# Optimization experiments

Hardware: AMD Instinct MI355X
Metric: run time of the kernel (lower is better)

Reference implementation:

```python
import jax, jax.numpy as jnp
from jax import lax
import numpy as np

B = 2; C = 128; H = 128; W = 128; NPIX = H * W
HTH = 184; HTW = 180; NBINS = HTH * HTW
NSPH = 16384; KHT = 8; KSPH = 16
N0, N1, N2 = 1024, 256, 64
K0, K1, K2 = 8, 8, 8
EPS = 1e-5


def setup_inputs() -> dict:
    key = jax.random.key(0)
    ks = jax.random.split(key, 24)
    f32 = jnp.float32
    inp = {}
    inp["image"] = jax.random.normal(ks[0], (B, C, H, W), f32)
    inp["bn_gamma"] = jnp.ones((C,), f32)
    inp["bn_beta"] = jnp.zeros((C,), f32)
    inp["ht_idx"] = jax.random.randint(ks[1], (NBINS, KHT), 0, NPIX, jnp.int32)
    inp["ht_w"] = jax.random.uniform(ks[2], (NBINS, KHT), f32)
    inp["w_htconv"] = jax.random.normal(ks[3], (3, 3, C, C), f32) / np.sqrt(9.0 * C)
    inp["htbn_gamma"] = jnp.ones((C,), f32)
    inp["htbn_beta"] = jnp.zeros((C,), f32)
    inp["sph_idx"] = jax.random.randint(ks[4], (NSPH, KSPH), 0, NBINS, jnp.int32)
    inp["sph_w"] = jax.random.uniform(ks[5], (NSPH, KSPH), f32)
    inp["w_sc"] = jax.random.normal(ks[6], (3, 64, C), f32) / np.sqrt(1.0 * C)
    inp["b_sc"] = jnp.zeros((3, 64), f32)
    inp["scbn_gamma"] = jnp.ones((3, 64), f32)
    inp["scbn_beta"] = jnp.zeros((3, 64), f32)
    inp["dgcn_w"] = jax.random.normal(ks[7], (3, 4, 128, 64), f32) / np.sqrt(128.0)
    inp["dgcn_b"] = jnp.zeros((3, 4, 64), f32)
    inp["dgcn_hw"] = jax.random.normal(ks[8], (3, 64), f32) / 8.0
    inp["dgcn_hb"] = jnp.zeros((3,), f32)
    inp["ind0"] = jax.random.randint(ks[9], (B, N0), 0, NSPH, jnp.int32)
    inp["ind1"] = jax.random.randint(ks[10], (B, 3, N1), 0, NSPH, jnp.int32)
    inp["ind2"] = jax.random.randint(ks[11], (B, 3, N2), 0, NSPH, jnp.int32)
    # kNN-style edges: structured centers (each node repeated k times), random neighbors
    c0 = jnp.tile(jnp.repeat(jnp.arange(N0, dtype=jnp.int32), K0)[None], (B, 1))
    inp["edge0"] = jnp.stack([c0, jax.random.randint(ks[12], (B, N0 * K0), 0, N0, jnp.int32)], 1)
    c1 = jnp.broadcast_to(jnp.repeat(jnp.arange(N1, dtype=jnp.int32), K1)[None, None], (B, 3, N1 * K1))
    inp["edge1"] = jnp.stack([c1, jax.random.randint(ks[13], (B, 3, N1 * K1), 0, N1, jnp.int32)], 2)
    c2 = jnp.broadcast_to(jnp.repeat(jnp.arange(N2, dtype=jnp.int32), K2)[None, None], (B, 3, N2 * K2))
    inp["edge2"] = jnp.stack([c2, jax.random.randint(ks[14], (B, 3, N2 * K2), 0, N2, jnp.int32)], 2)
    inp["target0"] = jax.random.randint(ks[15], (B, N0), 0, 2, jnp.int32)
    inp["target1"] = jax.random.randint(ks[16], (B * 3, N1), 0, 2, jnp.int32)
    inp["target2"] = jax.random.randint(ks[17], (B * 3, N2), 0, 2, jnp.int32)
    return inp


def _bn2d(x, g, b):
    m = x.mean((0, 2, 3), keepdims=True)
    v = x.var((0, 2, 3), keepdims=True)
    return g[None, :, None, None] * (x - m) * lax.rsqrt(v + EPS) + b[None, :, None, None]


def _sphere(x_htf, sph_idx, sph_w, ind):
    # x_htf: [B,C,NBINS]; ind: [B,S] -> weighted gather of HT bins per sphere node
    mi = sph_idx[ind]          # [B,S,K]
    mw = sph_w[ind]            # [B,S,K]
    g = jax.vmap(lambda xb, ib: xb[:, ib])(x_htf, mi)   # [B,C,S,K]
    return (g * mw[:, None]).sum(-1)                    # [B,C,S]


def _sconv(x, w, b, g, be):
    # 1x1 conv [B,C,S]->[B,64,S] + BN1d (batch stats) + ReLU
    y = jnp.einsum('oc,bcs->bos', w, x) + b[None, :, None]
    m = y.mean((0, 2), keepdims=True)
    v = y.var((0, 2), keepdims=True)
    return jax.nn.relu(g[None, :, None] * (y - m) * lax.rsqrt(v + EPS) + be[None, :, None])


def _dgcn(x, edge, ws, bs, hw, hb, n, k):
    # x: [Bg,n,64]; edge: [Bg,2,n*k] (row0=center, row1=neighbor); 4 EdgeConv layers
    for i in range(4):
        xc = jnp.take_along_axis(x, edge[:, 0, :, None], axis=1)   # [Bg,n*k,Cin]
        xn = jnp.take_along_axis(x, edge[:, 1, :, None], axis=1)
        h = jax.nn.relu(jnp.concatenate([xc, xn - xc], -1) @ ws[i] + bs[i])
        x = h.reshape(x.shape[0], n, k, -1).max(2)                 # max over neighbors
    return x @ hw + hb                                             # [Bg,n] logits


def _bce(logits, target):
    t = target.astype(logits.dtype)
    l = jnp.maximum(logits, 0.0) - logits * t + jnp.log1p(jnp.exp(-jnp.abs(logits)))
    pos = t > 0.5
    npos = jnp.maximum(pos.sum(), 1).astype(l.dtype)
    nneg = jnp.maximum((~pos).sum(), 1).astype(l.dtype)
    return jnp.where(pos, l, 0.0).sum() / npos, jnp.where(pos, 0.0, l).sum() / nneg


def _forward(image, bn_gamma, bn_beta, ht_idx, ht_w, w_htconv, htbn_gamma, htbn_beta,
             sph_idx, sph_w, w_sc, b_sc, scbn_gamma, scbn_beta,
             dgcn_w, dgcn_b, dgcn_hw, dgcn_hb,
             ind0, ind1, ind2, edge0, edge1, edge2, target0, target1, target2):
    x = jax.nn.relu(_bn2d(image, bn_gamma, bn_beta))
    xf = x.reshape(B, C, NPIX)
    # Hough voting: each HT bin accumulates KHT weighted pixels
    ht = (xf[:, :, ht_idx] * ht_w).sum(-1).reshape(B, C, HTH, HTW)
    hc = lax.conv_general_dilated(ht, w_htconv, (1, 1), 'SAME',
                                  dimension_numbers=('NCHW', 'HWIO', 'NCHW'))
    x_htf = jax.nn.relu(_bn2d(hc, htbn_gamma, htbn_beta)).reshape(B, C, NBINS)

    # scale 0
    x0 = _sconv(_sphere(x_htf, sph_idx, sph_w, ind0),
                w_sc[0], b_sc[0], scbn_gamma[0], scbn_beta[0]).transpose(0, 2, 1)
    x0 = _dgcn(x0, edge0, dgcn_w[0], dgcn_b[0], dgcn_hw[0], dgcn_hb[0], N0, K0)   # [B,N0]
    # scale 1 (3 vanishing-point branches folded into batch)
    x1 = _sconv(_sphere(x_htf, sph_idx, sph_w, ind1.reshape(B, -1)),
                w_sc[1], b_sc[1], scbn_gamma[1], scbn_beta[1]).transpose(0, 2, 1)
    x1 = _dgcn(x1.reshape(B * 3, N1, 64), edge1.reshape(B * 3, 2, N1 * K1),
               dgcn_w[1], dgcn_b[1], dgcn_hw[1], dgcn_hb[1], N1, K1)              # [B*3,N1]
    # scale 2
    x2 = _sconv(_sphere(x_htf, sph_idx, sph_w, ind2.reshape(B, -1)),
                w_sc[2], b_sc[2], scbn_gamma[2], scbn_beta[2]).transpose(0, 2, 1)
    x2 = _dgcn(x2.reshape(B * 3, N2, 64), edge2.reshape(B * 3, 2, N2 * K2),
               dgcn_w[2], dgcn_b[2], dgcn_hw[2], dgcn_hb[2], N2, K2)              # [B*3,N2]

    lp0, ln0 = _bce(x0, target0)
    lp1, ln1 = _bce(x1, target1)
    lp2, ln2 = _bce(x2, target2)
    losses = jnp.stack([lp0, ln0, lp1, ln1, lp2, ln2])
    preds = jnp.concatenate([jax.nn.sigmoid(x0).reshape(B, -1),
                             jax.nn.sigmoid(x1).reshape(B, -1),
                             jax.nn.sigmoid(x2).reshape(B, -1)], axis=1)
    return losses, preds


def reference(image, bn_gamma, bn_beta, ht_idx, ht_w, w_htconv, htbn_gamma, htbn_beta,
              sph_idx, sph_w, w_sc, b_sc, scbn_gamma, scbn_beta,
              dgcn_w, dgcn_b, dgcn_hw, dgcn_hb,
              ind0, ind1, ind2, edge0, edge1, edge2, target0, target1, target2):
    return _forward(image, bn_gamma, bn_beta, ht_idx, ht_w, w_htconv, htbn_gamma, htbn_beta,
                    sph_idx, sph_w, w_sc, b_sc, scbn_gamma, scbn_beta,
                    dgcn_w, dgcn_b, dgcn_hw, dgcn_hb,
                    ind0, ind1, ind2, edge0, edge1, edge2, target0, target1, target2)
```

## Files before the change

### kernel.cpp

```cpp
#include <hip/hip_runtime.h>
#include <math.h>

#define B_ 2
#define C_ 128
#define NPIX_ 16384
#define HTH_ 184
#define HTW_ 180
#define NBINS_ 33120
#define PH_ 186
#define PW_ 184
#define NPB_ 1984
#define TOTN_ 3968
#define EPS_ 1e-5f

#define ST_HC_SUM 0
#define ST_HC_SQ  128
#define ST_SC_SUM 256
#define ST_SC_SQ  448
#define ST_LOSS   640
#define ST_IMG_S1 1472
#define ST_IMG_S2 1600

typedef __attribute__((ext_vector_type(8))) short v8s;
typedef __attribute__((ext_vector_type(4))) float v4f;

__device__ inline unsigned short f2b(float f) {
  unsigned u = __builtin_bit_cast(unsigned, f);
  unsigned r = u + 0x7fffu + ((u >> 16) & 1u);
  return (unsigned short)(r >> 16);
}
__device__ inline float b2f(unsigned short u) {
  unsigned v = ((unsigned)u) << 16;
  return __builtin_bit_cast(float, v);
}

__global__ void kprep0(const float* __restrict__ w, const float* __restrict__ dw,
                       unsigned short* __restrict__ wtb, unsigned short* __restrict__ dwb,
                       unsigned* __restrict__ htb2, const float* __restrict__ img,
                       float* __restrict__ st) {
  int bid = blockIdx.x;
  int tid = threadIdx.x;
  if (bid < 1516) {
    int idx = bid*256 + tid;
    if (idx < 147456) {
      int tap = idx >> 14, z = idx & 16383;
      int j = z & 7, lane = (z >> 3) & 63, nt = (z >> 9) & 7, kt = (z >> 12) & 3;
      int l = lane & 15, q = lane >> 4;
      int co = nt*16 + l, ci = kt*32 + q*8 + j;
      wtb[idx] = f2b(w[(tap*C_ + ci)*C_ + co]);
    } else if (idx < 245760) {
      int i2 = idx - 147456;
      int sl = i2 >> 13, z = i2 & 8191;
      int j = z & 7, lane = (z >> 3) & 63, nt = (z >> 9) & 3, kt = (z >> 11) & 3;
      int l = lane & 15, q = lane >> 4;
      int co = nt*16 + l, cc = kt*32 + q*8 + j;
      dwb[i2] = f2b(dw[(sl*128 + cc)*64 + co]);
    } else if (idx < 388096) {
      int i = idx - 245760;
      int d = i & 63;
      int cell = i >> 6;
      int b = cell / 1112, j = cell % 1112;
      int y, x;
      if (j < 184) { y = 0; x = j; }
      else if (j < 368) { y = 185; x = j - 184; }
      else { int c = j - 368; int xi = c / 186; y = c % 186; x = xi == 0 ? 0 : 180 + xi; }
      htb2[((size_t)(b*PH_ + y)*PW_ + x)*64 + d] = 0u;
    }
  } else {
    int kb = bid - 1516;
    int c = kb >> 3, chunk = kb & 7;
    float s1 = 0.f, s2 = 0.f;
    for (int i = chunk*4096 + tid; i < (chunk+1)*4096; i += 256) {
      int b = i >> 14, p = i & (NPIX_-1);
      float v = img[((size_t)(b*C_ + c))*NPIX_ + p];
      s1 += v; s2 += v*v;
    }
    __shared__ float r1[256], r2[256];
    r1[tid] = s1; r2[tid] = s2; __syncthreads();
    for (int off = 128; off; off >>= 1) {
      if (tid < off) { r1[tid] += r1[tid+off]; r2[tid] += r2[tid+off]; }
      __syncthreads();
    }
    if (tid == 0) {
      atomicAdd(&st[ST_IMG_S1 + c], r1[0]);
      atomicAdd(&st[ST_IMG_S2 + c], r2[0]);
    }
  }
}

__global__ void k2_bnrelu_t(const float* __restrict__ img, const float* __restrict__ st,
                            const float* __restrict__ g, const float* __restrict__ be,
                            unsigned short* __restrict__ xt) {
  __shared__ float tile[32*65];
  __shared__ float ash[32], dsh[32];
  int p0 = blockIdx.x*64, c0 = blockIdx.y*32, b = blockIdx.z;
  int tid = threadIdx.x;
  if (tid < 32) {
    int c = c0 + tid;
    float n = (float)(B_*NPIX_);
    float m = st[ST_IMG_S1+c]/n;
    float var = st[ST_IMG_S2+c]/n - m*m;
    float a = g[c]*rsqrtf(var + EPS_);
    ash[tid] = a; dsh[tid] = be[c] - a*m;
  }
  __syncthreads();
  for (int r = 0; r < 8; r++) {
    int flat = tid + r*256;
    int row = flat >> 6, col = flat & 63;
    float v = img[((size_t)(b*C_ + c0 + row))*NPIX_ + p0 + col];
    tile[row*65 + col] = fmaxf(ash[row]*v + dsh[row], 0.f);
  }
  __syncthreads();
  for (int r = 0; r < 4; r++) {
    int flat = (tid + r*256)*2;
    int pl = flat >> 5, cl = flat & 31;
    unsigned lo = f2b(tile[cl*65 + pl]);
    unsigned hi = f2b(tile[(cl+1)*65 + pl]);
    *(unsigned*)&xt[((size_t)b*NPIX_ + p0 + pl)*C_ + c0 + cl] = lo | (hi << 16);
  }
}

__global__ void k3_hough(const unsigned* __restrict__ xt2, const int* __restrict__ hidx,
                         const float* __restrict__ hwt, unsigned* __restrict__ htb2) {
  int tid = threadIdx.x;
  int wv = __builtin_amdgcn_readfirstlane(tid >> 6);
  int bin = blockIdx.x*4 + wv;
  int b = blockIdx.y;
  int lane = tid & 63;
  const unsigned* base = xt2 + (size_t)b*NPIX_*64 + lane;
  float acc0 = 0.f, acc1 = 0.f;
  #pragma unroll
  for (int k = 0; k < 8; k++) {
    int p = hidx[bin*8 + k];
    float w = hwt[bin*8 + k];
    unsigned dv = base[(size_t)p*64];
    acc0 += w * b2f((unsigned short)(dv & 0xffff));
    acc1 += w * b2f((unsigned short)(dv >> 16));
  }
  int y = bin / HTW_, x = bin - y*HTW_;
  unsigned lo = f2b(acc0), hi = f2b(acc1);
  htb2[((size_t)(b*PH_ + y + 1)*PW_ + (x+1))*64 + lane] = lo | (hi << 16);
}

__global__ __launch_bounds__(256, 3) void k4_mfma(
    const unsigned short* __restrict__ htb, const unsigned short* __restrict__ wtb,
    unsigned short* __restrict__ hcb, float* __restrict__ st) {
  __shared__ char smem[32768];
  int tid = threadIdx.x;
  int wav = tid >> 6, lane = tid & 63;
  int quad = lane >> 4, l16 = lane & 15;
  int b = blockIdx.y;
  int p0 = blockIdx.x*128 + wav*32;
  size_t ab[2];
  #pragma unroll
  for (int t = 0; t < 2; t++) {
    int px = p0 + t*16 + l16; if (px > NBINS_-1) px = NBINS_-1;
    int y = px / HTW_, x = px % HTW_;
    ab[t] = (((size_t)(b*PH_ + y))*PW_ + x)*C_ + quad*8;
  }
  v4f acc[2][8];
  #pragma unroll
  for (int t = 0; t < 2; t++)
    #pragma unroll
    for (int nt = 0; nt < 8; nt++) acc[t][nt] = (v4f){0,0,0,0};

  for (int tap = 0; tap < 9; tap++) {
    __syncthreads();
    const uint4* src = (const uint4*)(wtb + tap*16384);
    uint4* dst = (uint4*)smem;
    #pragma unroll
    for (int s = 0; s < 8; s++) dst[tid + s*256] = src[tid + s*256];
    __syncthreads();
    int dy = tap/3, dx = tap - dy*3;
    int toff = (dy*PW_ + dx)*C_;
    v8s a[2][4];
    #pragma unroll
    for (int t = 0; t < 2; t++)
      #pragma unroll
      for (int kt = 0; kt < 4; kt++)
        a[t][kt] = *(const v8s*)&htb[ab[t] + toff + kt*32];
    #pragma unroll
    for (int kt = 0; kt < 4; kt++) {
      #pragma unroll
      for (int nt = 0; nt < 8; nt++) {
        v8s bf = *(const v8s*)(smem + ((((kt*8 + nt)*64) + lane) << 4));
        acc[0][nt] = __builtin_amdgcn_mfma_f32_16x16x32_bf16(a[0][kt], bf, acc[0][nt], 0, 0, 0);
        acc[1][nt] = __builtin_amdgcn_mfma_f32_16x16x32_bf16(a[1][kt], bf, acc[1][nt], 0, 0, 0);
      }
    }
  }
  __syncthreads();
  float* red = (float*)smem;
  float s1[8], s2[8];
  #pragma unroll
  for (int nt = 0; nt < 8; nt++) { s1[nt] = 0.f; s2[nt] = 0.f; }
  #pragma unroll
  for (int t = 0; t < 2; t++) {
    int pbase = p0 + t*16 + quad*4;
    #pragma unroll
    for (int nt = 0; nt < 8; nt++) {
      int co = nt*16 + l16;
      #pragma unroll
      for (int reg = 0; reg < 4; reg++) {
        int po = pbase + reg;
        if (po < NBINS_) {
          float v = acc[t][nt][reg];
          hcb[((size_t)b*NBINS_ + po)*C_ + co] = f2b(v);
          s1[nt] += v; s2[nt] += v*v;
        }
      }
    }
  }
  int slot = wav*4 + quad;
  #pragma unroll
  for (int nt = 0; nt < 8; nt++) red[(nt*16 + l16)*17 + slot] = s1[nt];
  __syncthreads();
  if (tid < 128) {
    float s = 0.f;
    #pragma unroll
    for (int k = 0; k < 16; k++) s += red[tid*17 + k];
    atomicAdd(&st[ST_HC_SUM + tid], s);
  }
  __syncthreads();
  #pragma unroll
  for (int nt = 0; nt < 8; nt++) red[(nt*16 + l16)*17 + slot] = s2[nt];
  __syncthreads();
  if (tid < 128) {
    float s = 0.f;
    #pragma unroll
    for (int k = 0; k < 16; k++) s += red[tid*17 + k];
    atomicAdd(&st[ST_HC_SQ + tid], s);
  }
}

__global__ __launch_bounds__(256) void k67_sphconv(
    const unsigned* __restrict__ hcb2, const float* __restrict__ g, const float* __restrict__ be,
    const int* __restrict__ sph_idx, const float* __restrict__ sph_w,
    const int* __restrict__ ind0, const int* __restrict__ ind1, const int* __restrict__ ind2,
    const float* __restrict__ w_sc, const float* __restrict__ b_sc,
    float* __restrict__ y, float* __restrict__ st) {
  __shared__ float xs[32*128];
  __shared__ float wT[128*65];
  __shared__ float red[256];
  int tid = threadIdx.x;
  int gn0 = blockIdx.x*32;
  int nb0 = gn0 % NPB_;
  int s = nb0 < 1024 ? 0 : (nb0 < 1792 ? 1 : 2);
  int wv = tid >> 6, lane = tid & 63;
  {
    int c0 = lane*2, c1 = c0 + 1;
    float n = (float)(B_*NBINS_);
    float m0 = st[ST_HC_SUM + c0]/n, m1 = st[ST_HC_SUM + c1]/n;
    float va0 = st[ST_HC_SQ + c0]/n - m0*m0, va1 = st[ST_HC_SQ + c1]/n - m1*m1;
    float a0 = g[c0]*rsqrtf(va0 + EPS_), a1 = g[c1]*rsqrtf(va1 + EPS_);
    float d0 = be[c0] - a0*m0, d1 = be[c1] - a1*m1;
    for (int i = 0; i < 8; i++) {
      int node_l = wv*8 + i;
      int gn = gn0 + node_l;
      int b = gn / NPB_, nb = gn % NPB_;
      int v;
      if (nb < 1024) v = ind0[b*1024 + nb];
      else if (nb < 1792) v = ind1[b*768 + nb - 1024];
      else v = ind2[b*192 + nb - 1792];
      v = __builtin_amdgcn_readfirstlane(v);
      const unsigned* base = hcb2 + (size_t)b*NBINS_*64 + lane;
      float acc0 = 0.f, acc1 = 0.f;
      #pragma unroll
      for (int k = 0; k < 16; k++) {
        int mi = sph_idx[v*16 + k];
        float mw = sph_w[v*16 + k];
        unsigned dv = base[(size_t)mi*64];
        acc0 += mw * fmaxf(a0*b2f((unsigned short)(dv & 0xffff)) + d0, 0.f);
        acc1 += mw * fmaxf(a1*b2f((unsigned short)(dv >> 16)) + d1, 0.f);
      }
      *(float2*)&xs[node_l*128 + c0] = make_float2(acc0, acc1);
    }
  }
  for (int r = 0; r < 32; r++) {
    int flat = tid + r*256;
    int o = flat >> 7, cc = flat & 127;
    wT[cc*65 + o] = w_sc[(s*64 + o)*C_ + cc];
  }
  __syncthreads();
  int o = tid & 63, nl = tid >> 6;
  float bias = b_sc[s*64 + o];
  float acc[8];
  #pragma unroll
  for (int i = 0; i < 8; i++) acc[i] = bias;
  for (int cc = 0; cc < 128; cc++) {
    float wvv = wT[cc*65 + o];
    #pragma unroll
    for (int i = 0; i < 8; i++)
      acc[i] += xs[(nl*8 + i)*128 + cc] * wvv;
  }
  float s1 = 0.f, s2 = 0.f;
  #pragma unroll
  for (int i = 0; i < 8; i++) {
    y[(size_t)(gn0 + nl*8 + i)*64 + o] = acc[i];
    s1 += acc[i]; s2 += acc[i]*acc[i];
  }
  red[tid] = s1; __syncthreads();
  if (nl == 0) atomicAdd(&st[ST_SC_SUM + s*64 + o], red[o] + red[64+o] + red[128+o] + red[192+o]);
  __syncthreads();
  red[tid] = s2; __syncthreads();
  if (nl == 0) atomicAdd(&st[ST_SC_SQ + s*64 + o], red[o] + red[64+o] + red[128+o] + red[192+o]);
}

__global__ __launch_bounds__(256) void k10_dgcn(
    const void* __restrict__ xin_, unsigned short* __restrict__ xout,
    const int* __restrict__ edge0, const int* __restrict__ edge1, const int* __restrict__ edge2,
    const unsigned short* __restrict__ dwb, const float* __restrict__ db,
    const float* __restrict__ st, const float* __restrict__ scg, const float* __restrict__ scb,
    int layer, int usebn) {
  __shared__ unsigned short E[128*136];
  __shared__ float ash[64], dsh[64];
  int tid = threadIdx.x;
  int bid = blockIdx.x;
  int s, node_base, le_blk, span; const int* ec;
  if (bid < 128) {
    s = 0; int b = bid >> 6; node_base = b*NPB_; le_blk = (bid & 63)*128;
    span = 8192; ec = edge0 + b*2*8192;
  } else if (bid < 224) {
    int j = bid - 128; s = 1; int seg = j >> 4; int b = seg/3, vp = seg%3;
    node_base = b*NPB_ + 1024 + vp*256; le_blk = (j & 15)*128;
    span = 2048; ec = edge1 + ((b*3+vp)*2)*2048;
  } else {
    int j = bid - 224; s = 2; int seg = j >> 2; int b = seg/3, vp = seg%3;
    node_base = b*NPB_ + 1792 + vp*64; le_blk = (j & 3)*128;
    span = 512; ec = edge2 + ((b*3+vp)*2)*512;
  }
  const int* en = ec + span;
  if (usebn) {
    if (tid < 64) {
      float n = s==0 ? 2048.f : (s==1 ? 1536.f : 384.f);
      float m = st[ST_SC_SUM + s*64 + tid]/n;
      float var = st[ST_SC_SQ + s*64 + tid]/n - m*m;
      float a = scg[s*64 + tid]*rsqrtf(var + EPS_);
      ash[tid] = a; dsh[tid] = scb[s*64 + tid] - a*m;
    }
    __syncthreads();
  }
  {
    int r = tid >> 1, h = tid & 1;
    int e = le_blk + r;
    int ci = ec[e], ni = en[e];
    if (usebn) {
      const float* xc = (const float*)xin_ + (size_t)(node_base + ci)*64;
      const float* xn = (const float*)xin_ + (size_t)(node_base + ni)*64;
      #pragma unroll
      for (int c8 = 0; c8 < 64; c8 += 8) {
        v8s pk;
        #pragma unroll
        for (int j = 0; j < 8; j++) {
          int c = c8 + j;
          float vc = fmaxf(ash[c]*xc[c] + dsh[c], 0.f);
          float val = vc;
          if (h) val = fmaxf(ash[c]*xn[c] + dsh[c], 0.f) - vc;
          pk[j] = (short)f2b(val);
        }
        *(v8s*)&E[r*136 + h*64 + c8] = pk;
      }
    } else {
      const unsigned short* xc = (const unsigned short*)xin_ + (size_t)(node_base + ci)*64;
      const unsigned short* xn = (const unsigned short*)xin_ + (size_t)(node_base + ni)*64;
      #pragma unroll
      for (int c8 = 0; c8 < 64; c8 += 8) {
        v8s vc8 = *(const v8s*)&xc[c8];
        v8s pk = vc8;
        if (h) {
          v8s vn8 = *(const v8s*)&xn[c8];
          #pragma unroll
          for (int j = 0; j < 8; j++)
            pk[j] = (short)f2b(b2f((unsigned short)vn8[j]) - b2f((unsigned short)vc8[j]));
        }
        *(v8s*)&E[r*136 + h*64 + c8] = pk;
      }
    }
  }
  __syncthreads();
  int wave = tid >> 6, lane = tid & 63;
  int quad = lane >> 4, l16 = lane & 15;
  const unsigned short* wb = dwb + (size_t)(s*4 + layer)*8192;
  v4f acc[2][4];
  #pragma unroll
  for (int t = 0; t < 2; t++)
    #pragma unroll
    for (int nt = 0; nt < 4; nt++) acc[t][nt] = (v4f){0,0,0,0};
  #pragma unroll
  for (int kt = 0; kt < 4; kt++) {
    v8s a0 = *(const v8s*)&E[(wave*32 + l16)*136 + quad*8 + kt*32];
    v8s a1 = *(const v8s*)&E[(wave*32 + 16 + l16)*136 + quad*8 + kt*32];
    #pragma unroll
    for (int nt = 0; nt < 4; nt++) {
      v8s bf = *(const v8s*)&wb[((kt*4 + nt)*64 + lane)*8];
      acc[0][nt] = __builtin_amdgcn_mfma_f32_16x16x32_bf16(a0, bf, acc[0][nt], 0, 0, 0);
      acc[1][nt] = __builtin_amdgcn_mfma_f32_16x16x32_bf16(a1, bf, acc[1][nt], 0, 0, 0);
    }
  }
  int vb0 = le_blk/8 + wave*4;
  #pragma unroll
  for (int t = 0; t < 2; t++) {
    #pragma unroll
    for (int nt = 0; nt < 4; nt++) {
      float bias = db[(s*4 + layer)*64 + nt*16 + l16];
      float m = fmaxf(fmaxf(acc[t][nt][0], acc[t][nt][1]),
                      fmaxf(acc[t][nt][2], acc[t][nt][3]));
      m = fmaxf(m + bias, 0.f);
      float other = __shfl_xor(m, 16);
      m = fmaxf(m, other);
      if ((quad & 1) == 0) {
        int v = vb0 + t*2 + (quad >> 1);
        xout[(size_t)(node_base + v)*64 + nt*16 + l16] = f2b(m);
      }
    }
  }
}

__global__ __launch_bounds__(256) void k11_head(
    const unsigned short* __restrict__ x, const float* __restrict__ hw, const float* __restrict__ hb,
    const int* __restrict__ t0, const int* __restrict__ t1, const int* __restrict__ t2,
    float* __restrict__ out, float* __restrict__ st) {
  __shared__ float shw[192];
  int tid = threadIdx.x;
  if (tid < 192) shw[tid] = hw[tid];
  __syncthreads();
  int gn = blockIdx.x*256 + tid;
  bool valid = gn < TOTN_;
  int g = valid ? gn : TOTN_-1;
  int b = g / NPB_, nb = g % NPB_;
  int s, tg;
  if (nb < 1024) { s = 0; tg = t0[b*1024 + nb]; }
  else if (nb < 1792) { s = 1; int j = nb-1024; tg = t1[(b*3 + (j>>8))*256 + (j&255)]; }
  else { s = 2; int j = nb-1792; tg = t2[(b*3 + (j>>6))*64 + (j&63)]; }
  const unsigned short* row = x + (size_t)g*64;
  float logit = hb[s];
  #pragma unroll
  for (int c8 = 0; c8 < 64; c8 += 8) {
    v8s v = *(const v8s*)&row[c8];
    #pragma unroll
    for (int j = 0; j < 8; j++)
      logit += b2f((unsigned short)v[j]) * shw[s*64 + c8 + j];
  }
  if (valid) out[6 + gn] = 1.f / (1.f + expf(-logit));
  float tf = (float)tg;
  float l = fmaxf(logit, 0.f) - logit*tf + log1pf(expf(-fabsf(logit)));
  float sp = (valid && tg) ? l : 0.f;
  float sn = (valid && !tg) ? l : 0.f;
  float cp = (valid && tg) ? 1.f : 0.f;
  float cn = (valid && !tg) ? 1.f : 0.f;
  for (int off = 32; off; off >>= 1) {
    sp += __shfl_down(sp, off);
    sn += __shfl_down(sn, off);
    cp += __shfl_down(cp, off);
    cn += __shfl_down(cn, off);
  }
  if ((tid & 63) == 0) {
    atomicAdd(&st[ST_LOSS + s*4 + 0], sp);
    atomicAdd(&st[ST_LOSS + s*4 + 1], sn);
    atomicAdd(&st[ST_LOSS + s*4 + 2], cp);
    atomicAdd(&st[ST_LOSS + s*4 + 3], cn);
  }
}

__global__ void k12_fin(const float* __restrict__ st, float* __restrict__ out) {
  int i = threadIdx.x;
  if (i < 6) {
    int s = i >> 1; int pos = !(i & 1);
    float sum = st[ST_LOSS + s*4 + (pos ? 0 : 1)];
    float cnt = st[ST_LOSS + s*4 + (pos ? 2 : 3)];
    out[i] = sum / fmaxf(cnt, 1.f);
  }
}

extern "C" void kernel_launch(void* const* d_in, const int* in_sizes, int n_in,
                              void* d_out, int out_size, void* d_ws, size_t ws_size,
                              hipStream_t stream) {
  const float* image  = (const float*)d_in[0];
  const float* bn_g   = (const float*)d_in[1];
  const float* bn_b   = (const float*)d_in[2];
  const int*   ht_idx = (const int*)  d_in[3];
  const float* ht_w   = (const float*)d_in[4];
  const float* w_conv = (const float*)d_in[5];
  const float* htbn_g = (const float*)d_in[6];
  const float* htbn_b = (const float*)d_in[7];
  const int*   sph_idx= (const int*)  d_in[8];
  const float* sph_w  = (const float*)d_in[9];
  const float* w_sc   = (const float*)d_in[10];
  const float* b_sc   = (const float*)d_in[11];
  const float* scbn_g = (const float*)d_in[12];
  const float* scbn_b = (const float*)d_in[13];
  const float* dgcn_w = (const float*)d_in[14];
  const float* dgcn_b = (const float*)d_in[15];
  const float* dgcn_hw= (const float*)d_in[16];
  const float* dgcn_hb= (const float*)d_in[17];
  const int*   ind0   = (const int*)  d_in[18];
  const int*   ind1   = (const int*)  d_in[19];
  const int*   ind2   = (const int*)  d_in[20];
  const int*   edge0  = (const int*)  d_in[21];
  const int*   edge1  = (const int*)  d_in[22];
  const int*   edge2  = (const int*)  d_in[23];
  const int*   t0     = (const int*)  d_in[24];
  const int*   t1     = (const int*)  d_in[25];
  const int*   t2     = (const int*)  d_in[26];
  float* out = (float*)d_out;

  char* ws = (char*)d_ws;
  unsigned short* x_t   = (unsigned short*)(ws);
  unsigned short* htb   = (unsigned short*)(ws +  8388608);
  unsigned short* hcb   = (unsigned short*)(ws + 25911296);
  unsigned short* wtb   = (unsigned short*)(ws + 42868736);
  unsigned short* dwb   = (unsigned short*)(ws + 43163648);
  float*          y_sc  = (float*)(ws + 43360256);
  unsigned short* xdgA  = (unsigned short*)(ws + 44376064);
  unsigned short* xdgB  = (unsigned short*)(ws + 44883968);
  float*          st    = (float*)(ws + 45391872);

  hipMemsetAsync(st, 0, 1728*sizeof(float), stream);
  kprep0<<<2540, 256, 0, stream>>>(w_conv, dgcn_w, wtb, dwb, (unsigned*)htb, image, st);
  k2_bnrelu_t<<<dim3(256,4,2), 256, 0, stream>>>(image, st, bn_g, bn_b, x_t);
  k3_hough<<<dim3(NBINS_/4, B_), 256, 0, stream>>>((const unsigned*)x_t, ht_idx, ht_w, (unsigned*)htb);
  k4_mfma<<<dim3(259, 2), 256, 0, stream>>>(htb, wtb, hcb, st);
  k67_sphconv<<<TOTN_/32, 256, 0, stream>>>((const unsigned*)hcb, htbn_g, htbn_b, sph_idx, sph_w,
                                            ind0, ind1, ind2, w_sc, b_sc, y_sc, st);
  k10_dgcn<<<248, 256, 0, stream>>>((const void*)y_sc, xdgA, edge0, edge1, edge2, dwb, dgcn_b, st, scbn_g, scbn_b, 0, 1);
  k10_dgcn<<<248, 256, 0, stream>>>((const void*)xdgA, xdgB, edge0, edge1, edge2, dwb, dgcn_b, st, scbn_g, scbn_b, 1, 0);
  k10_dgcn<<<248, 256, 0, stream>>>((const void*)xdgB, xdgA, edge0, edge1, edge2, dwb, dgcn_b, st, scbn_g, scbn_b, 2, 0);
  k10_dgcn<<<248, 256, 0, stream>>>((const void*)xdgA, xdgB, edge0, edge1, edge2, dwb, dgcn_b, st, scbn_g, scbn_b, 3, 0);
  k11_head<<<16, 256, 0, stream>>>(xdgB, dgcn_hw, dgcn_hb, t0, t1, t2, out, st);
  k12_fin<<<1, 64, 0, stream>>>(st, out);
}
```

Before: 249.3 us.

## Use MFMA for sphere conv, double-buffer conv weights, split DGCN blocks finer

Several separate changes. The sphere-conv linear layer moves from an FP32 shared-memory loop to bf16 MFMA, using weights pre-packed in the prep kernel, with 8 nodes per block instead of 32. The Hough conv kernel now double-buffers per-tap weights in 64KB of shared memory, prefetching the next tap through registers so each tap needs only one barrier. The DGCN kernel halves edges per block, doubling the grid, and loads inputs as float4. These aim to cut scalar FMA work, barrier stalls and underfilled grids, at the cost of lower occupancy in the conv kernel and reduced bf16 precision in sphere conv.

```diff
diff --git a/kernel.cpp b/kernel.cpp
--- a/kernel.cpp
+++ b/kernel.cpp
@@ -35,12 +35,14 @@
 }
 
 __global__ void kprep0(const float* __restrict__ w, const float* __restrict__ dw,
+                       const float* __restrict__ wsc,
                        unsigned short* __restrict__ wtb, unsigned short* __restrict__ dwb,
+                       unsigned short* __restrict__ swb,
                        unsigned* __restrict__ htb2, const float* __restrict__ img,
                        float* __restrict__ st) {
   int bid = blockIdx.x;
   int tid = threadIdx.x;
-  if (bid < 1516) {
+  if (bid < 1612) {
     int idx = bid*256 + tid;
     if (idx < 147456) {
       int tap = idx >> 14, z = idx & 16383;
@@ -55,8 +57,15 @@
       int l = lane & 15, q = lane >> 4;
       int co = nt*16 + l, cc = kt*32 + q*8 + j;
       dwb[i2] = f2b(dw[(sl*128 + cc)*64 + co]);
-    } else if (idx < 388096) {
-      int i = idx - 245760;
+    } else if (idx < 270336) {
+      int i3 = idx - 245760;
+      int s = i3 >> 13, z = i3 & 8191;
+      int j = z & 7, lane = (z >> 3) & 63, nt = (z >> 9) & 3, kt = (z >> 11) & 3;
+      int l = lane & 15, q = lane >> 4;
+      int co = nt*16 + l, cc = kt*32 + q*8 + j;
+      swb[i3] = f2b(wsc[(s*64 + co)*128 + cc]);
+    } else if (idx < 412672) {
+      int i = idx - 270336;
       int d = i & 63;
       int cell = i >> 6;
       int b = cell / 1112, j = cell % 1112;
@@ -67,7 +76,7 @@
       htb2[((size_t)(b*PH_ + y)*PW_ + x)*64 + d] = 0u;
     }
   } else {
-    int kb = bid - 1516;
+    int kb = bid - 1612;
     int c = kb >> 3, chunk = kb & 7;
     float s1 = 0.f, s2 = 0.f;
     for (int i = chunk*4096 + tid; i < (chunk+1)*4096; i += 256) {
@@ -142,10 +151,10 @@
   htb2[((size_t)(b*PH_ + y + 1)*PW_ + (x+1))*64 + lane] = lo | (hi << 16);
 }
 
-__global__ __launch_bounds__(256, 3) void k4_mfma(
+__global__ __launch_bounds__(256) void k4_mfma(
     const unsigned short* __restrict__ htb, const unsigned short* __restrict__ wtb,
     unsigned short* __restrict__ hcb, float* __restrict__ st) {
-  __shared__ char smem[32768];
+  __shared__ char smem[65536];
   int tid = threadIdx.x;
   int wav = tid >> 6, lane = tid & 63;
   int quad = lane >> 4, l16 = lane & 15;
@@ -164,13 +173,21 @@
     #pragma unroll
     for (int nt = 0; nt < 8; nt++) acc[t][nt] = (v4f){0,0,0,0};
 
+  {
+    const uint4* src = (const uint4*)wtb;
+    uint4* dst = (uint4*)smem;
+    #pragma unroll
+    for (int s = 0; s < 8; s++) dst[tid + s*256] = src[tid + s*256];
+  }
+  __syncthreads();
   for (int tap = 0; tap < 9; tap++) {
-    __syncthreads();
-    const uint4* src = (const uint4*)(wtb + tap*16384);
-    uint4* dst = (uint4*)smem;
-    #pragma unroll
-    for (int s = 0; s < 8; s++) dst[tid + s*256] = src[tid + s*256];
-    __syncthreads();
+    uint4 wreg[8];
+    if (tap < 8) {
+      const uint4* src = (const uint4*)(wtb + (tap+1)*16384);
+      #pragma unroll
+      for (int s = 0; s < 8; s++) wreg[s] = src[tid + s*256];
+    }
+    const char* cur = smem + (tap & 1)*32768;
     int dy = tap/3, dx = tap - dy*3;
     int toff = (dy*PW_ + dx)*C_;
     v8s a[2][4];
@@ -183,13 +200,18 @@
     for (int kt = 0; kt < 4; kt++) {
       #pragma unroll
       for (int nt = 0; nt < 8; nt++) {
-        v8s bf = *(const v8s*)(smem + ((((kt*8 + nt)*64) + lane) << 4));
+        v8s bf = *(const v8s*)(cur + ((((kt*8 + nt)*64) + lane) << 4));
         acc[0][nt] = __builtin_amdgcn_mfma_f32_16x16x32_bf16(a[0][kt], bf, acc[0][nt], 0, 0, 0);
         acc[1][nt] = __builtin_amdgcn_mfma_f32_16x16x32_bf16(a[1][kt], bf, acc[1][nt], 0, 0, 0);
       }
     }
-  }
-  __syncthreads();
+    if (tap < 8) {
+      uint4* dst = (uint4*)(smem + ((tap+1) & 1)*32768);
+      #pragma unroll
+      for (int s = 0; s < 8; s++) dst[tid + s*256] = wreg[s];
+    }
+    __syncthreads();
+  }
   float* red = (float*)smem;
   float s1[8], s2[8];
   #pragma unroll
@@ -237,16 +259,15 @@
     const unsigned* __restrict__ hcb2, const float* __restrict__ g, const float* __restrict__ be,
     const int* __restrict__ sph_idx, const float* __restrict__ sph_w,
     const int* __restrict__ ind0, const int* __restrict__ ind1, const int* __restrict__ ind2,
-    const float* __restrict__ w_sc, const float* __restrict__ b_sc,
+    const unsigned short* __restrict__ swb, const float* __restrict__ b_sc,
     float* __restrict__ y, float* __restrict__ st) {
-  __shared__ float xs[32*128];
-  __shared__ float wT[128*65];
-  __shared__ float red[256];
-  int tid = threadIdx.x;
-  int gn0 = blockIdx.x*32;
+  __shared__ unsigned short E[16*136];
+  int tid = threadIdx.x;
+  int gn0 = blockIdx.x*8;
   int nb0 = gn0 % NPB_;
   int s = nb0 < 1024 ? 0 : (nb0 < 1792 ? 1 : 2);
   int wv = tid >> 6, lane = tid & 63;
+  int quad = lane >> 4, l16 = lane & 15;
   {
     int c0 = lane*2, c1 = c0 + 1;
     float n = (float)(B_*NBINS_);
@@ -254,8 +275,9 @@
     float va0 = st[ST_HC_SQ + c0]/n - m0*m0, va1 = st[ST_HC_SQ + c1]/n - m1*m1;
     float a0 = g[c0]*rsqrtf(va0 + EPS_), a1 = g[c1]*rsqrtf(va1 + EPS_);
     float d0 = be[c0] - a0*m0, d1 = be[c1] - a1*m1;
-    for (int i = 0; i < 8; i++) {
-      int node_l = wv*8 + i;
+    #pragma unroll
+    for (int i = 0; i < 2; i++) {
+      int node_l = wv*2 + i;
       int gn = gn0 + node_l;
       int b = gn / NPB_, nb = gn % NPB_;
       int v;
@@ -273,37 +295,36 @@
         acc0 += mw * fmaxf(a0*b2f((unsigned short)(dv & 0xffff)) + d0, 0.f);
         acc1 += mw * fmaxf(a1*b2f((unsigned short)(dv >> 16)) + d1, 0.f);
       }
-      *(float2*)&xs[node_l*128 + c0] = make_float2(acc0, acc1);
-    }
-  }
-  for (int r = 0; r < 32; r++) {
-    int flat = tid + r*256;
-    int o = flat >> 7, cc = flat & 127;
-    wT[cc*65 + o] = w_sc[(s*64 + o)*C_ + cc];
-  }
-  __syncthreads();
-  int o = tid & 63, nl = tid >> 6;
-  float bias = b_sc[s*64 + o];
-  float acc[8];
-  #pragma unroll
-  for (int i = 0; i < 8; i++) acc[i] = bias;
-  for (int cc = 0; cc < 128; cc++) {
-    float wvv = wT[cc*65 + o];
-    #pragma unroll
-    for (int i = 0; i < 8; i++)
-      acc[i] += xs[(nl*8 + i)*128 + cc] * wvv;
-  }
+      unsigned lo = f2b(acc0), hi = f2b(acc1);
+      *(unsigned*)&E[node_l*136 + c0] = lo | (hi << 16);
+    }
+  }
+  __syncthreads();
+  v4f acc = (v4f){0,0,0,0};
+  const unsigned short* wb = swb + s*8192 + wv*512;
+  #pragma unroll
+  for (int kt = 0; kt < 4; kt++) {
+    v8s a = *(const v8s*)&E[l16*136 + quad*8 + kt*32];
+    v8s bf = *(const v8s*)&wb[kt*2048 + lane*8];
+    acc = __builtin_amdgcn_mfma_f32_16x16x32_bf16(a, bf, acc, 0, 0, 0);
+  }
+  float bias = b_sc[s*64 + wv*16 + l16];
   float s1 = 0.f, s2 = 0.f;
   #pragma unroll
-  for (int i = 0; i < 8; i++) {
-    y[(size_t)(gn0 + nl*8 + i)*64 + o] = acc[i];
-    s1 += acc[i]; s2 += acc[i]*acc[i];
-  }
-  red[tid] = s1; __syncthreads();
-  if (nl == 0) atomicAdd(&st[ST_SC_SUM + s*64 + o], red[o] + red[64+o] + red[128+o] + red[192+o]);
-  __syncthreads();
-  red[tid] = s2; __syncthreads();
-  if (nl == 0) atomicAdd(&st[ST_SC_SQ + s*64 + o], red[o] + red[64+o] + red[128+o] + red[192+o]);
+  for (int reg = 0; reg < 4; reg++) {
+    int row = quad*4 + reg;
+    if (quad < 2) {
+      float val = acc[reg] + bias;
+      y[(size_t)(gn0 + row)*64 + wv*16 + l16] = val;
+      s1 += val; s2 += val*val;
+    }
+  }
+  s1 += __shfl_xor(s1, 16);
+  s2 += __shfl_xor(s2, 16);
+  if (quad == 0) {
+    atomicAdd(&st[ST_SC_SUM + s*64 + wv*16 + l16], s1);
+    atomicAdd(&st[ST_SC_SQ  + s*64 + wv*16 + l16], s2);
+  }
 }
 
 __global__ __launch_bounds__(256) void k10_dgcn(
@@ -312,21 +333,21 @@
     const unsigned short* __restrict__ dwb, const float* __restrict__ db,
     const float* __restrict__ st, const float* __restrict__ scg, const float* __restrict__ scb,
     int layer, int usebn) {
-  __shared__ unsigned short E[128*136];
+  __shared__ unsigned short E[64*136];
   __shared__ float ash[64], dsh[64];
   int tid = threadIdx.x;
   int bid = blockIdx.x;
   int s, node_base, le_blk, span; const int* ec;
-  if (bid < 128) {
-    s = 0; int b = bid >> 6; node_base = b*NPB_; le_blk = (bid & 63)*128;
+  if (bid < 256) {
+    s = 0; int b = bid >> 7; node_base = b*NPB_; le_blk = (bid & 127)*64;
     span = 8192; ec = edge0 + b*2*8192;
-  } else if (bid < 224) {
-    int j = bid - 128; s = 1; int seg = j >> 4; int b = seg/3, vp = seg%3;
-    node_base = b*NPB_ + 1024 + vp*256; le_blk = (j & 15)*128;
+  } else if (bid < 448) {
+    int j = bid - 256; s = 1; int seg = j >> 5; int b = seg/3, vp = seg%3;
+    node_base = b*NPB_ + 1024 + vp*256; le_blk = (j & 31)*64;
     span = 2048; ec = edge1 + ((b*3+vp)*2)*2048;
   } else {
-    int j = bid - 224; s = 2; int seg = j >> 2; int b = seg/3, vp = seg%3;
-    node_base = b*NPB_ + 1792 + vp*64; le_blk = (j & 3)*128;
+    int j = bid - 448; s = 2; int seg = j >> 3; int b = seg/3, vp = seg%3;
+    node_base = b*NPB_ + 1792 + vp*64; le_blk = (j & 7)*64;
     span = 512; ec = edge2 + ((b*3+vp)*2)*512;
   }
   const int* en = ec + span;
@@ -341,30 +362,43 @@
     __syncthreads();
   }
   {
-    int r = tid >> 1, h = tid & 1;
-    int e = le_blk + r;
+    int e_l = tid >> 2, part = tid & 3;
+    int h = part >> 1, cb = (part & 1)*32;
+    int e = le_blk + e_l;
     int ci = ec[e], ni = en[e];
     if (usebn) {
-      const float* xc = (const float*)xin_ + (size_t)(node_base + ci)*64;
-      const float* xn = (const float*)xin_ + (size_t)(node_base + ni)*64;
-      #pragma unroll
-      for (int c8 = 0; c8 < 64; c8 += 8) {
+      const float* xc = (const float*)xin_ + (size_t)(node_base + ci)*64 + cb;
+      const float* xn = (const float*)xin_ + (size_t)(node_base + ni)*64 + cb;
+      float4 xc4[8], xn4[8];
+      #pragma unroll
+      for (int q = 0; q < 8; q++) xc4[q] = *(const float4*)&xc[q*4];
+      if (h) {
+        #pragma unroll
+        for (int q = 0; q < 8; q++) xn4[q] = *(const float4*)&xn[q*4];
+      }
+      #pragma unroll
+      for (int c8 = 0; c8 < 32; c8 += 8) {
         v8s pk;
         #pragma unroll
         for (int j = 0; j < 8; j++) {
-          int c = c8 + j;
-          float vc = fmaxf(ash[c]*xc[c] + dsh[c], 0.f);
+          int cl = c8 + j;
+          int c = cb + cl;
+          float xcv = ((const float*)xc4)[cl];
+          float vc = fmaxf(ash[c]*xcv + dsh[c], 0.f);
           float val = vc;
-          if (h) val = fmaxf(ash[c]*xn[c] + dsh[c], 0.f) - vc;
+          if (h) {
+            float xnv = ((const float*)xn4)[cl];
+            val = fmaxf(ash[c]*xnv + dsh[c], 0.f) - vc;
+          }
           pk[j] = (short)f2b(val);
         }
-        *(v8s*)&E[r*136 + h*64 + c8] = pk;
+        *(v8s*)&E[e_l*136 + h*64 + cb + c8] = pk;
       }
     } else {
-      const unsigned short* xc = (const unsigned short*)xin_ + (size_t)(node_base + ci)*64;
-      const unsigned short* xn = (const unsigned short*)xin_ + (size_t)(node_base + ni)*64;
-      #pragma unroll
-      for (int c8 = 0; c8 < 64; c8 += 8) {
+      const unsigned short* xc = (const unsigned short*)xin_ + (size_t)(node_base + ci)*64 + cb;
+      const unsigned short* xn = (const unsigned short*)xin_ + (size_t)(node_base + ni)*64 + cb;
+      #pragma unroll
+      for (int c8 = 0; c8 < 32; c8 += 8) {
         v8s vc8 = *(const v8s*)&xc[c8];
         v8s pk = vc8;
         if (h) {
@@ -373,7 +407,7 @@
           for (int j = 0; j < 8; j++)
             pk[j] = (short)f2b(b2f((unsigned short)vn8[j]) - b2f((unsigned short)vc8[j]));
         }
-        *(v8s*)&E[r*136 + h*64 + c8] = pk;
+        *(v8s*)&E[e_l*136 + h*64 + cb + c8] = pk;
       }
     }
   }
@@ -381,37 +415,28 @@
   int wave = tid >> 6, lane = tid & 63;
   int quad = lane >> 4, l16 = lane & 15;
   const unsigned short* wb = dwb + (size_t)(s*4 + layer)*8192;
-  v4f acc[2][4];
-  #pragma unroll
-  for (int t = 0; t < 2; t++)
-    #pragma unroll
-    for (int nt = 0; nt < 4; nt++) acc[t][nt] = (v4f){0,0,0,0};
+  v4f acc[4];
+  #pragma unroll
+  for (int nt = 0; nt < 4; nt++) acc[nt] = (v4f){0,0,0,0};
   #pragma unroll
   for (int kt = 0; kt < 4; kt++) {
-    v8s a0 = *(const v8s*)&E[(wave*32 + l16)*136 + quad*8 + kt*32];
-    v8s a1 = *(const v8s*)&E[(wave*32 + 16 + l16)*136 + quad*8 + kt*32];
+    v8s a = *(const v8s*)&E[(wave*16 + l16)*136 + quad*8 + kt*32];
     #pragma unroll
     for (int nt = 0; nt < 4; nt++) {
       v8s bf = *(const v8s*)&wb[((kt*4 + nt)*64 + lane)*8];
-      acc[0][nt] = __builtin_amdgcn_mfma_f32_16x16x32_bf16(a0, bf, acc[0][nt], 0, 0, 0);
-      acc[1][nt] = __builtin_amdgcn_mfma_f32_16x16x32_bf16(a1, bf, acc[1][nt], 0, 0, 0);
-    }
-  }
-  int vb0 = le_blk/8 + wave*4;
-  #pragma unroll
-  for (int t = 0; t < 2; t++) {
-    #pragma unroll
-    for (int nt = 0; nt < 4; nt++) {
-      float bias = db[(s*4 + layer)*64 + nt*16 + l16];
-      float m = fmaxf(fmaxf(acc[t][nt][0], acc[t][nt][1]),
-                      fmaxf(acc[t][nt][2], acc[t][nt][3]));
-      m = fmaxf(m + bias, 0.f);
-      float other = __shfl_xor(m, 16);
-      m = fmaxf(m, other);
-      if ((quad & 1) == 0) {
-        int v = vb0 + t*2 + (quad >> 1);
-        xout[(size_t)(node_base + v)*64 + nt*16 + l16] = f2b(m);
-      }
+      acc[nt] = __builtin_amdgcn_mfma_f32_16x16x32_bf16(a, bf, acc[nt], 0, 0, 0);
+    }
+  }
+  #pragma unroll
+  for (int nt = 0; nt < 4; nt++) {
+    float bias = db[(s*4 + layer)*64 + nt*16 + l16];
+    float m = fmaxf(fmaxf(acc[nt][0], acc[nt][1]), fmaxf(acc[nt][2], acc[nt][3]));
+    m = fmaxf(m + bias, 0.f);
+    float other = __shfl_xor(m, 16);
+    m = fmaxf(m, other);
+    if ((quad & 1) == 0) {
+      int node_l = wave*2 + (quad >> 1);
+      xout[(size_t)(node_base + (le_blk >> 3) + node_l)*64 + nt*16 + l16] = f2b(m);
     }
   }
 }
@@ -510,22 +535,23 @@
   unsigned short* hcb   = (unsigned short*)(ws + 25911296);
   unsigned short* wtb   = (unsigned short*)(ws + 42868736);
   unsigned short* dwb   = (unsigned short*)(ws + 43163648);
-  float*          y_sc  = (float*)(ws + 43360256);
-  unsigned short* xdgA  = (unsigned short*)(ws + 44376064);
-  unsigned short* xdgB  = (unsigned short*)(ws + 44883968);
-  float*          st    = (float*)(ws + 45391872);
+  unsigned short* swb   = (unsigned short*)(ws + 43360256);
+  float*          y_sc  = (float*)(ws + 43409408);
+  unsigned short* xdgA  = (unsigned short*)(ws + 44425216);
+  unsigned short* xdgB  = (unsigned short*)(ws + 44933120);
+  float*          st    = (float*)(ws + 45441024);
 
   hipMemsetAsync(st, 0, 1728*sizeof(float), stream);
-  kprep0<<<2540, 256, 0, stream>>>(w_conv, dgcn_w, wtb, dwb, (unsigned*)htb, image, st);
+  kprep0<<<2636, 256, 0, stream>>>(w_conv, dgcn_w, w_sc, wtb, dwb, swb, (unsigned*)htb, image, st);
   k2_bnrelu_t<<<dim3(256,4,2), 256, 0, stream>>>(image, st, bn_g, bn_b, x_t);
   k3_hough<<<dim3(NBINS_/4, B_), 256, 0, stream>>>((const unsigned*)x_t, ht_idx, ht_w, (unsigned*)htb);
   k4_mfma<<<dim3(259, 2), 256, 0, stream>>>(htb, wtb, hcb, st);
-  k67_sphconv<<<TOTN_/32, 256, 0, stream>>>((const unsigned*)hcb, htbn_g, htbn_b, sph_idx, sph_w,
-                                            ind0, ind1, ind2, w_sc, b_sc, y_sc, st);
-  k10_dgcn<<<248, 256, 0, stream>>>((const void*)y_sc, xdgA, edge0, edge1, edge2, dwb, dgcn_b, st, scbn_g, scbn_b, 0, 1);
-  k10_dgcn<<<248, 256, 0, stream>>>((const void*)xdgA, xdgB, edge0, edge1, edge2, dwb, dgcn_b, st, scbn_g, scbn_b, 1, 0);
-  k10_dgcn<<<248, 256, 0, stream>>>((const void*)xdgB, xdgA, edge0, edge1, edge2, dwb, dgcn_b, st, scbn_g, scbn_b, 2, 0);
-  k10_dgcn<<<248, 256, 0, stream>>>((const void*)xdgA, xdgB, edge0, edge1, edge2, dwb, dgcn_b, st, scbn_g, scbn_b, 3, 0);
+  k67_sphconv<<<TOTN_/8, 256, 0, stream>>>((const unsigned*)hcb, htbn_g, htbn_b, sph_idx, sph_w,
+                                           ind0, ind1, ind2, swb, b_sc, y_sc, st);
+  k10_dgcn<<<496, 256, 0, stream>>>((const void*)y_sc, xdgA, edge0, edge1, edge2, dwb, dgcn_b, st, scbn_g, scbn_b, 0, 1);
+  k10_dgcn<<<496, 256, 0, stream>>>((const void*)xdgA, xdgB, edge0, edge1, edge2, dwb, dgcn_b, st, scbn_g, scbn_b, 1, 0);
+  k10_dgcn<<<496, 256, 0, stream>>>((const void*)xdgB, xdgA, edge0, edge1, edge2, dwb, dgcn_b, st, scbn_g, scbn_b, 2, 0);
+  k10_dgcn<<<496, 256, 0, stream>>>((const void*)xdgA, xdgB, edge0, edge1, edge2, dwb, dgcn_b, st, scbn_g, scbn_b, 3, 0);
   k11_head<<<16, 256, 0, stream>>>(xdgB, dgcn_hw, dgcn_hb, t0, t1, t2, out, st);
   k12_fin<<<1, 64, 0, stream>>>(st, out);
 }
```

Result: faster. 241.7 us (-3.0%).
